# Kernel optimization log

Hardware: AMD Instinct MI355X
Metric: run time of the kernel (lower is better)

## Reference

```python
import jax, jax.numpy as jnp
import numpy as np

P = 16  # patch_size

def setup_inputs() -> dict:
    key = jax.random.key(0)
    k1, k2, k3, k4, k5 = jax.random.split(key, 5)
    B, C, H, W = 8, 256, 256, 256
    x = jax.random.normal(k1, (B, C, H, W), dtype=jnp.float32)
    w1 = jax.random.normal(k2, (C, C), dtype=jnp.float32) * 0.02
    b1 = jax.random.normal(k3, (C,), dtype=jnp.float32) * 0.02
    w2 = jax.random.normal(k4, (C, C), dtype=jnp.float32) * 0.02
    b2 = jax.random.normal(k5, (C,), dtype=jnp.float32) * 0.02
    return {"x": x, "w1": w1, "b1": b1, "w2": w2, "b2": b2}

def reference(x, w1, b1, w2, b2):
    B, C, H, W = x.shape
    h, w = H // P, W // P
    # global feature: mean over all spatial positions -> (B, C)
    gf = jnp.mean(x, axis=(2, 3))
    # local features: per-patch mean -> (B, C, h, w)
    lf = jnp.mean(x.reshape(B, C, h, P, w, P), axis=(3, 5))
    lf = lf.reshape(B, C, h * w).transpose(0, 2, 1)  # (B, hw, C)
    mix = jnp.concatenate([lf, gf[:, None, :]], axis=1)  # (B, hw+1, C)
    m = jax.nn.relu(jnp.einsum('bnc,oc->bno', mix, w1) + b1)
    m = jax.nn.relu(jnp.einsum('bnc,oc->bno', m, w2) + b2)
    lf2, gf2 = m[:, :-1, :], m[:, -1, :]  # (B, hw, C), (B, C)
    scores = jnp.einsum('bnc,bc->bn', lf2, gf2)  # (B, hw)
    att = jax.nn.softmax(scores, axis=1).reshape(B, 1, h, w)
    # upsample attention over each patch (nearest / block-broadcast)
    att_up = jnp.repeat(jnp.repeat(att, P, axis=2), P, axis=3)  # (B,1,H,W)
    return x + x * att_up
```

## Files before the change

### kernel.cpp

```cpp
#include <hip/hip_runtime.h>
#include <hip/hip_bf16.h>

#define WS_W1T 0
#define WS_W2T 65536
#define WS_MIX 131072
#define WS_M2  657408
#define WS_ATT 1183744

__global__ void k_transpose(const float* __restrict__ w1,
                            const float* __restrict__ w2,
                            float* __restrict__ w1t,
                            float* __restrict__ w2t) {
    int t = blockIdx.x * 256 + threadIdx.x;
    int idx = t & 65535;
    int o = idx >> 8, c = idx & 255;
    if (t < 65536) w1t[c * 256 + o] = w1[idx];
    else           w2t[c * 256 + o] = w2[idx];
}

__global__ void k_patch_means(const float* __restrict__ x,
                              float* __restrict__ mix) {
    int plane = blockIdx.x;
    int b = plane >> 8, c = plane & 255;
    const float4* p = (const float4*)x + (size_t)plane * 16384;
    int t = threadIdx.x;
    int lane = t & 63, wid = t >> 6;
    int pcol = lane >> 2;

    __shared__ float bins[16][17];
    bins[t >> 4][t & 15] = 0.f;
    __syncthreads();

    float acc = 0.f;
    #pragma unroll 4
    for (int it = 0; it < 64; ++it) {
        int row = it * 4 + wid;
        float4 v = p[row * 64 + lane];
        acc += v.x + v.y + v.z + v.w;
        if ((it & 3) == 3) {
            acc += __shfl_xor(acc, 1);
            acc += __shfl_xor(acc, 2);
            if ((lane & 3) == 0) atomicAdd(&bins[it >> 2][pcol], acc);
            acc = 0.f;
        }
    }
    __syncthreads();

    float pm = bins[t >> 4][t & 15] * (1.0f / 256.0f);
    mix[((size_t)b * 257 + t) * 256 + c] = pm;

    float s = pm;
    for (int off = 1; off < 64; off <<= 1) s += __shfl_xor(s, off);
    __shared__ float wsum[4];
    if (lane == 0) wsum[wid] = s;
    __syncthreads();
    if (t == 0) {
        float g = (wsum[0] + wsum[1] + wsum[2] + wsum[3]) * (1.0f / 256.0f);
        mix[((size_t)b * 257 + 256) * 256 + c] = g;
    }
}

__global__ void k_mlp(const float* __restrict__ mix,
                      const float* __restrict__ w1t, const float* __restrict__ b1,
                      const float* __restrict__ w2t, const float* __restrict__ b2,
                      float* __restrict__ m2out) {
    int r0 = blockIdx.x * 4;
    int o = threadIdx.x;

    __shared__ float in[4][256];
    __shared__ float mid[4][256];
    #pragma unroll
    for (int j = 0; j < 4; ++j) in[j][o] = mix[(size_t)(r0 + j) * 256 + o];
    __syncthreads();

    float acc[4];
    float bb = b1[o];
    #pragma unroll
    for (int j = 0; j < 4; ++j) acc[j] = bb;
    #pragma unroll 4
    for (int c = 0; c < 256; ++c) {
        float wv = w1t[c * 256 + o];
        #pragma unroll
        for (int j = 0; j < 4; ++j) acc[j] = fmaf(in[j][c], wv, acc[j]);
    }
    #pragma unroll
    for (int j = 0; j < 4; ++j) mid[j][o] = fmaxf(acc[j], 0.f);
    __syncthreads();

    float bb2 = b2[o];
    #pragma unroll
    for (int j = 0; j < 4; ++j) acc[j] = bb2;
    #pragma unroll 4
    for (int c = 0; c < 256; ++c) {
        float wv = w2t[c * 256 + o];
        #pragma unroll
        for (int j = 0; j < 4; ++j) acc[j] = fmaf(mid[j][c], wv, acc[j]);
    }
    #pragma unroll
    for (int j = 0; j < 4; ++j)
        m2out[(size_t)(r0 + j) * 256 + o] = fmaxf(acc[j], 0.f);
}

__global__ void k_softmax(const float* __restrict__ m2,
                          float* __restrict__ att) {
    int b = blockIdx.x;
    const float* base = m2 + (size_t)b * 257 * 256;
    int t = threadIdx.x, lane = t & 63, wid = t >> 6;

    __shared__ float gf2[256];
    gf2[t] = base[256 * 256 + t];
    __syncthreads();

    const float* rowp = base + (size_t)t * 256;
    float s = 0.f;
    #pragma unroll 4
    for (int c = 0; c < 256; ++c) s = fmaf(rowp[c], gf2[c], s);

    float m = s;
    for (int off = 1; off < 64; off <<= 1) m = fmaxf(m, __shfl_xor(m, off));
    __shared__ float red[4];
    if (lane == 0) red[wid] = m;
    __syncthreads();
    m = fmaxf(fmaxf(red[0], red[1]), fmaxf(red[2], red[3]));

    float e = __expf(s - m);
    float sum = e;
    for (int off = 1; off < 64; off <<= 1) sum += __shfl_xor(sum, off);
    __shared__ float red2[4];
    __syncthreads();
    if (lane == 0) red2[wid] = sum;
    __syncthreads();
    sum = red2[0] + red2[1] + red2[2] + red2[3];

    att[b * 256 + t] = e / sum;
}

__global__ void k_apply(const float* __restrict__ x,
                        const float* __restrict__ att,
                        float* __restrict__ out) {
    size_t i = (size_t)blockIdx.x * 256 + threadIdx.x;
    const float4* xv = (const float4*)x;
    float4* ov = (float4*)out;
    int plane = (int)(i >> 14);
    int j = (int)(i & 16383);
    int row = j >> 6, col4 = j & 63;
    int patch = ((row >> 4) << 4) | (col4 >> 2);
    int b = plane >> 8;
    float a = 1.0f + att[(b << 8) + patch];
    float4 v = xv[i];
    v.x *= a; v.y *= a; v.z *= a; v.w *= a;
    ov[i] = v;
}

extern "C" void kernel_launch(void* const* d_in, const int* in_sizes, int n_in,
                              void* d_out, int out_size, void* d_ws, size_t ws_size,
                              hipStream_t stream) {
    const float* x  = (const float*)d_in[0];
    const float* w1 = (const float*)d_in[1];
    const float* b1 = (const float*)d_in[2];
    const float* w2 = (const float*)d_in[3];
    const float* b2 = (const float*)d_in[4];
    float* out = (float*)d_out;
    float* ws  = (float*)d_ws;

    float* w1t = ws + WS_W1T;
    float* w2t = ws + WS_W2T;
    float* mix = ws + WS_MIX;
    float* m2  = ws + WS_M2;
    float* att = ws + WS_ATT;

    k_transpose<<<512, 256, 0, stream>>>(w1, w2, w1t, w2t);
    k_patch_means<<<8 * 256, 256, 0, stream>>>(x, mix);
    k_mlp<<<(8 * 257) / 4, 256, 0, stream>>>(mix, w1t, b1, w2t, b2, m2);
    k_softmax<<<8, 256, 0, stream>>>(m2, att);
    k_apply<<<(8 * 256 * 256 * 256 / 4) / 256, 256, 0, stream>>>(x, att, out);
}
```

Measured before the change: 362.1 us.

## Streamline patch means, softmax scoring, and apply with nontemporal vector access

Patch-mean reduction drops shared-memory atomics and bin zeroing. Each wave now sums one contiguous 16-row band per patch row and writes bins directly. Softmax scoring uses 1024 threads with one wave per row, doing a coalesced vector dot product plus shuffle reduction instead of strided per-thread row reads. The apply kernel handles four vectors per thread, and both streaming kernels use nontemporal loads and stores to reduce cache pollution on the large input. This targets the memory-bound passes and the poorly coalesced, low-parallelism softmax, at the cost of fewer blocks in apply and more synchronisation-heavy 1024-thread blocks.

```diff
diff --git a/kernel.cpp b/kernel.cpp
--- a/kernel.cpp
+++ b/kernel.cpp
@@ -1,5 +1,7 @@
 #include <hip/hip_runtime.h>
 #include <hip/hip_bf16.h>
+
+typedef float f32x4 __attribute__((ext_vector_type(4)));
 
 #define WS_W1T 0
 #define WS_W2T 65536
@@ -22,27 +24,24 @@
                               float* __restrict__ mix) {
     int plane = blockIdx.x;
     int b = plane >> 8, c = plane & 255;
-    const float4* p = (const float4*)x + (size_t)plane * 16384;
+    const f32x4* p = (const f32x4*)x + (size_t)plane * 16384;
     int t = threadIdx.x;
     int lane = t & 63, wid = t >> 6;
     int pcol = lane >> 2;
 
-    __shared__ float bins[16][17];
-    bins[t >> 4][t & 15] = 0.f;
-    __syncthreads();
+    __shared__ float bins[16][16];
 
-    float acc = 0.f;
-    #pragma unroll 4
-    for (int it = 0; it < 64; ++it) {
-        int row = it * 4 + wid;
-        float4 v = p[row * 64 + lane];
-        acc += v.x + v.y + v.z + v.w;
-        if ((it & 3) == 3) {
-            acc += __shfl_xor(acc, 1);
-            acc += __shfl_xor(acc, 2);
-            if ((lane & 3) == 0) atomicAdd(&bins[it >> 2][pcol], acc);
-            acc = 0.f;
+    const f32x4* wp = p + (size_t)wid * 64 * 64 + lane;
+    for (int band = 0; band < 4; ++band) {
+        float acc = 0.f;
+        #pragma unroll
+        for (int r = 0; r < 16; ++r) {
+            f32x4 v = __builtin_nontemporal_load(wp + (band * 16 + r) * 64);
+            acc += v.x + v.y + v.z + v.w;
         }
+        acc += __shfl_xor(acc, 1);
+        acc += __shfl_xor(acc, 2);
+        if ((lane & 3) == 0) bins[wid * 4 + band][pcol] = acc;
     }
     __syncthreads();
 
@@ -105,51 +104,65 @@
                           float* __restrict__ att) {
     int b = blockIdx.x;
     const float* base = m2 + (size_t)b * 257 * 256;
-    int t = threadIdx.x, lane = t & 63, wid = t >> 6;
+    int t = threadIdx.x;
+    int lane = t & 63, w = t >> 6;
 
     __shared__ float gf2[256];
-    gf2[t] = base[256 * 256 + t];
+    __shared__ float scores[256];
+    if (t < 256) gf2[t] = base[65536 + t];
     __syncthreads();
 
-    const float* rowp = base + (size_t)t * 256;
-    float s = 0.f;
-    #pragma unroll 4
-    for (int c = 0; c < 256; ++c) s = fmaf(rowp[c], gf2[c], s);
+    f32x4 gv = ((const f32x4*)gf2)[lane];
+    for (int r = 0; r < 16; ++r) {
+        int n = w * 16 + r;
+        f32x4 v = ((const f32x4*)(base + (size_t)n * 256))[lane];
+        float s = v.x * gv.x + v.y * gv.y + v.z * gv.z + v.w * gv.w;
+        #pragma unroll
+        for (int off = 1; off < 64; off <<= 1) s += __shfl_xor(s, off);
+        if (lane == 0) scores[n] = s;
+    }
+    __syncthreads();
 
+    float s = (t < 256) ? scores[t] : -1e30f;
     float m = s;
+    #pragma unroll
     for (int off = 1; off < 64; off <<= 1) m = fmaxf(m, __shfl_xor(m, off));
-    __shared__ float red[4];
-    if (lane == 0) red[wid] = m;
+    __shared__ float redm[16];
+    if (lane == 0) redm[w] = m;
     __syncthreads();
-    m = fmaxf(fmaxf(red[0], red[1]), fmaxf(red[2], red[3]));
+    float M = fmaxf(fmaxf(redm[0], redm[1]), fmaxf(redm[2], redm[3]));
 
-    float e = __expf(s - m);
+    float e = (t < 256) ? __expf(s - M) : 0.f;
     float sum = e;
+    #pragma unroll
     for (int off = 1; off < 64; off <<= 1) sum += __shfl_xor(sum, off);
-    __shared__ float red2[4];
+    __shared__ float reds[16];
+    if (lane == 0) reds[w] = sum;
     __syncthreads();
-    if (lane == 0) red2[wid] = sum;
-    __syncthreads();
-    sum = red2[0] + red2[1] + red2[2] + red2[3];
+    float S = reds[0] + reds[1] + reds[2] + reds[3];
 
-    att[b * 256 + t] = e / sum;
+    if (t < 256) att[b * 256 + t] = e / S;
 }
 
 __global__ void k_apply(const float* __restrict__ x,
                         const float* __restrict__ att,
                         float* __restrict__ out) {
-    size_t i = (size_t)blockIdx.x * 256 + threadIdx.x;
-    const float4* xv = (const float4*)x;
-    float4* ov = (float4*)out;
-    int plane = (int)(i >> 14);
-    int j = (int)(i & 16383);
-    int row = j >> 6, col4 = j & 63;
-    int patch = ((row >> 4) << 4) | (col4 >> 2);
-    int b = plane >> 8;
-    float a = 1.0f + att[(b << 8) + patch];
-    float4 v = xv[i];
-    v.x *= a; v.y *= a; v.z *= a; v.w *= a;
-    ov[i] = v;
+    const f32x4* xv = (const f32x4*)x;
+    f32x4* ov = (f32x4*)out;
+    size_t base = (size_t)blockIdx.x * 1024 + threadIdx.x;
+    #pragma unroll
+    for (int k = 0; k < 4; ++k) {
+        size_t i = base + (size_t)k * 256;
+        int plane = (int)(i >> 14);
+        int j = (int)(i & 16383);
+        int row = j >> 6, col4 = j & 63;
+        int patch = ((row >> 4) << 4) | (col4 >> 2);
+        int b = plane >> 8;
+        float a = 1.0f + att[(b << 8) + patch];
+        f32x4 v = __builtin_nontemporal_load(&xv[i]);
+        v.x *= a; v.y *= a; v.z *= a; v.w *= a;
+        __builtin_nontemporal_store(v, &ov[i]);
+    }
 }
 
 extern "C" void kernel_launch(void* const* d_in, const int* in_sizes, int n_in,
@@ -172,6 +185,6 @@
     k_transpose<<<512, 256, 0, stream>>>(w1, w2, w1t, w2t);
     k_patch_means<<<8 * 256, 256, 0, stream>>>(x, mix);
     k_mlp<<<(8 * 257) / 4, 256, 0, stream>>>(mix, w1t, b1, w2t, b2, m2);
-    k_softmax<<<8, 256, 0, stream>>>(m2, att);
-    k_apply<<<(8 * 256 * 256 * 256 / 4) / 256, 256, 0, stream>>>(x, att, out);
+    k_softmax<<<8, 1024, 0, stream>>>(m2, att);
+    k_apply<<<32768, 256, 0, stream>>>(x, att, out);
 }
```

Result: faster. 315.4 us (-12.9%).
